# Kernel optimization log

Hardware: AMD Instinct MI355X
Metric: run time of the kernel (lower is better)

## Reference

```python
import jax, jax.numpy as jnp
import numpy as np

UAV_DIM, TASK_DIM = 32, 32
E, H, HID = 128, 4, 256
B, U, T = 16, 64, 128
ENC_H = 128  # encoder hidden width


def _mlp3(x, w0, b0, w1, b1, w2, b2):
    # Linear->ReLU->Linear->ReLU->Linear (weights stored as (in,out))
    x = jax.nn.relu(x @ w0 + b0)
    x = jax.nn.relu(x @ w1 + b1)
    return x @ w2 + b2


def setup_inputs() -> dict:
    key = jax.random.key(0)
    ks = jax.random.split(key, 20)
    s = lambda fan_in: 1.0 / np.sqrt(fan_in)
    d = {
        'uav_feat': jax.random.normal(ks[0], (B, U, UAV_DIM), jnp.float32),
        'task_feat': jax.random.normal(ks[1], (B, T, TASK_DIM), jnp.float32),
        # UAV encoder
        'uw0': jax.random.normal(ks[2], (UAV_DIM, ENC_H), jnp.float32) * s(UAV_DIM),
        'ub0': jnp.zeros((ENC_H,), jnp.float32),
        'uw1': jax.random.normal(ks[3], (ENC_H, ENC_H), jnp.float32) * s(ENC_H),
        'ub1': jnp.zeros((ENC_H,), jnp.float32),
        'uw2': jax.random.normal(ks[4], (ENC_H, E), jnp.float32) * s(ENC_H),
        'ub2': jnp.zeros((E,), jnp.float32),
        # Task encoder
        'tw0': jax.random.normal(ks[5], (TASK_DIM, ENC_H), jnp.float32) * s(TASK_DIM),
        'tb0': jnp.zeros((ENC_H,), jnp.float32),
        'tw1': jax.random.normal(ks[6], (ENC_H, ENC_H), jnp.float32) * s(ENC_H),
        'tb1': jnp.zeros((ENC_H,), jnp.float32),
        'tw2': jax.random.normal(ks[7], (ENC_H, E), jnp.float32) * s(ENC_H),
        'tb2': jnp.zeros((E,), jnp.float32),
        # head queries + fusion MLP (fw1 is the (2E,HID) first linear)
        'head_q': jax.random.normal(ks[8], (H, E), jnp.float32),
        'fw1': jax.random.normal(ks[9], (2 * E, HID), jnp.float32) * s(2 * E),
        'fb1': jnp.zeros((HID,), jnp.float32),
        'fw2': jax.random.normal(ks[10], (HID, 1), jnp.float32) * s(HID),
        'fb2': jnp.zeros((1,), jnp.float32),
    }
    return d


def reference(uav_feat, task_feat, uw0, ub0, uw1, ub1, uw2, ub2,
              tw0, tb0, tw1, tb1, tw2, tb2, head_q, fw1, fb1, fw2, fb2):
    ue = _mlp3(uav_feat, uw0, ub0, uw1, ub1, uw2, ub2)   # (B,U,E)
    te = _mlp3(task_feat, tw0, tb0, tw1, tb1, tw2, tb2)  # (B,T,E)
    # q = uav_embed + per-head query: (B,H,U,E)
    q = ue[:, None, :, :] + head_q[None, :, None, :]
    # Split cat([q,k]) @ fw1 into q@fw1[:E] + k@fw1[E:] — same math, no 2E concat
    qh = jnp.einsum('bhue,ed->bhud', q, fw1[:E])          # (B,H,U,HID)
    kh = jnp.einsum('bte,ed->btd', te, fw1[E:])           # (B,T,HID)
    pre = qh[:, :, :, None, :] + kh[:, None, None, :, :] + fb1  # (B,H,U,T,HID)
    h = jax.nn.relu(pre)
    logits = jnp.einsum('bhutd,do->bhuto', h, fw2)[..., 0] + fb2[0]  # (B,H,U,T)
    return logits
```

## Files before the change

### kernel.cpp

```cpp
#include <hip/hip_runtime.h>
#include <hip/hip_bf16.h>

#define B_ 16
#define U_ 64
#define T_ 128
#define H_ 4
#define E_ 128
#define HID_ 256

typedef _Float16 half_t;
typedef _Float16 h2 __attribute__((ext_vector_type(2)));

__device__ __forceinline__ h2 u2h(unsigned u){ h2 r; __builtin_memcpy(&r, &u, 4); return r; }
__device__ __forceinline__ unsigned pkh(float a, float b){
  h2 r; r.x = (_Float16)a; r.y = (_Float16)b;
  unsigned u; __builtin_memcpy(&u, &r, 4); return u;
}

#define ENC_R 8

__device__ __forceinline__ void layer128(const float (*in)[128], float (*out)[128],
    const float* __restrict__ W, const float* __restrict__ Bb, int j, bool do_relu)
{
  float a[ENC_R];
  float bb = Bb[j];
  #pragma unroll
  for (int r=0;r<ENC_R;r++) a[r]=bb;
  #pragma unroll
  for (int ic=0; ic<4; ic++){
    float w[32];
    #pragma unroll
    for (int i=0;i<32;i++) w[i]=W[(ic*32+i)*128 + j];
    #pragma unroll
    for (int r=0;r<ENC_R;r++){
      float s=0.f;
      #pragma unroll
      for (int i=0;i<32;i++) s = fmaf(in[r][ic*32+i], w[i], s);
      a[r]+=s;
    }
  }
  #pragma unroll
  for (int r=0;r<ENC_R;r++) out[r][j] = do_relu ? fmaxf(a[r],0.f) : a[r];
}

__global__ __launch_bounds__(128) void enc_kernel(
  const float* __restrict__ uav, const float* __restrict__ task,
  const float* __restrict__ uw0, const float* __restrict__ ub0,
  const float* __restrict__ uw1, const float* __restrict__ ub1,
  const float* __restrict__ uw2, const float* __restrict__ ub2,
  const float* __restrict__ tw0, const float* __restrict__ tb0,
  const float* __restrict__ tw1, const float* __restrict__ tb1,
  const float* __restrict__ tw2, const float* __restrict__ tb2,
  const float* __restrict__ headq, const float* __restrict__ fw1,
  float* __restrict__ ueW, half_t* __restrict__ Kg, float* __restrict__ QhW)
{
  __shared__ float X[ENC_R][32];
  __shared__ float Ha[ENC_R][128];
  __shared__ float Hb[ENC_R][128];
  const int j = threadIdx.x;
  const int blk = blockIdx.x;

  const float *w0=nullptr,*b0=nullptr,*w1=nullptr,*b1=nullptr,*w2=nullptr,*b2=nullptr,*xin=nullptr;
  const float* fwbase;
  float* outF = nullptr;
  half_t* outB = nullptr;
  bool only_last = false;
  int row0;

  if (blk < 128) {
    row0 = blk*ENC_R;
    xin = uav + row0*32;
    w0=uw0;b0=ub0;w1=uw1;b1=ub1;w2=uw2;b2=ub2;
    fwbase = fw1;
    outF = ueW + row0*HID_;
  } else if (blk < 384) {
    row0 = (blk-128)*ENC_R;
    xin = task + row0*32;
    w0=tw0;b0=tb0;w1=tw1;b1=tb1;w2=tw2;b2=tb2;
    fwbase = fw1 + 128*HID_;
    outB = Kg + row0*HID_;
  } else {
    only_last = true;
    fwbase = fw1;
    outF = QhW;
  }

  if (!only_last) {
    for (int idx=j; idx<ENC_R*32; idx+=128){ int r=idx>>5, i=idx&31; X[r][i]=xin[idx]; }
    __syncthreads();
    {
      float w[32];
      #pragma unroll
      for (int i=0;i<32;i++) w[i]=w0[i*128 + j];
      float bb=b0[j];
      #pragma unroll
      for (int r=0;r<ENC_R;r++){
        float a=bb;
        #pragma unroll
        for (int i=0;i<32;i++) a = fmaf(X[r][i], w[i], a);
        Ha[r][j]=fmaxf(a,0.f);
      }
    }
    __syncthreads();
    layer128(Ha,Hb,w1,b1,j,true);
    __syncthreads();
    layer128(Hb,Ha,w2,b2,j,false);
    __syncthreads();
  } else {
    #pragma unroll
    for (int r=0;r<4;r++) Ha[r][j] = headq[r*128 + j];
    __syncthreads();
  }

  #pragma unroll
  for (int o=0;o<2;o++){
    const int jo = o*128 + j;
    float a[ENC_R];
    #pragma unroll
    for (int r=0;r<ENC_R;r++) a[r]=0.f;
    #pragma unroll
    for (int ic=0; ic<4; ic++){
      float w[32];
      #pragma unroll
      for (int i=0;i<32;i++) w[i]=fwbase[(ic*32+i)*HID_ + jo];
      #pragma unroll
      for (int r=0;r<ENC_R;r++){
        float s=0.f;
        #pragma unroll
        for (int i=0;i<32;i++) s = fmaf(Ha[r][ic*32+i], w[i], s);
        a[r]+=s;
      }
    }
    if (!only_last) {
      if (outF) {
        #pragma unroll
        for (int r=0;r<ENC_R;r++) outF[r*HID_ + jo] = a[r];
      } else {
        #pragma unroll
        for (int r=0;r<ENC_R;r++) outB[r*HID_ + jo] = (half_t)a[r];
      }
    } else {
      #pragma unroll
      for (int r=0;r<4;r++) outF[r*HID_ + jo] = a[r];
    }
  }
}

#define UTILE 8

__global__ __launch_bounds__(256) void logits_kernel(
  const float* __restrict__ ueW, const float* __restrict__ QhW,
  const half_t* __restrict__ Kg,
  const float* __restrict__ fb1, const float* __restrict__ fw2,
  const float* __restrict__ fb2, float* __restrict__ out)
{
  __shared__ uint4 Kl4[64*32];
  __shared__ uint4 baseb[UTILE][32];
  __shared__ uint4 w2b[32];

  const int tid = threadIdx.x;
  const int wv = tid >> 6;
  const int lane = tid & 63;
  const int b = blockIdx.z, h = blockIdx.y;
  const int u0 = blockIdx.x * UTILE;

  {
    const int u = tid >> 5;
    const int c = tid & 31;
    const float4* ue4 = (const float4*)(ueW + (b*U_ + u0 + u)*HID_);
    const float4* q4  = (const float4*)(QhW + h*HID_);
    const float4* f4  = (const float4*)fb1;
    float4 a0 = ue4[2*c],   a1 = ue4[2*c+1];
    float4 b0 = q4[2*c],    b1 = q4[2*c+1];
    float4 c0 = f4[2*c],    c1 = f4[2*c+1];
    uint4 pv;
    pv.x = pkh(a0.x+b0.x+c0.x, a0.y+b0.y+c0.y);
    pv.y = pkh(a0.z+b0.z+c0.z, a0.w+b0.w+c0.w);
    pv.z = pkh(a1.x+b1.x+c1.x, a1.y+b1.y+c1.y);
    pv.w = pkh(a1.z+b1.z+c1.z, a1.w+b1.w+c1.w);
    baseb[u][c] = pv;
    if (tid < 32) {
      const float4* w4 = (const float4*)fw2;
      float4 w0 = w4[2*tid], w1 = w4[2*tid+1];
      uint4 wv4;
      wv4.x = pkh(w0.x, w0.y); wv4.y = pkh(w0.z, w0.w);
      wv4.z = pkh(w1.x, w1.y); wv4.w = pkh(w1.z, w1.w);
      w2b[tid] = wv4;
    }
  }
  const float fb2f = fb2[0];
  const uint4* Kgp = (const uint4*)(Kg + (size_t)b*T_*HID_);

  const int r0 = wv*2;
  const h2 hz = (h2)((_Float16)0);

  for (int s=0; s<2; s++){
    const int t0 = s*64;
    if (s) __syncthreads();
    for (int i = tid; i < 64*32; i += 256){
      const int t = i >> 5, c = i & 31;
      Kl4[t*32 + ((c + t)&31)] = Kgp[(t0 + t)*32 + c];
    }
    __syncthreads();
    const uint4* myrow = Kl4 + lane*32;
    float acc0 = 0.f, acc1 = 0.f;
    #pragma unroll
    for (int c=0; c<32; c++){
      const uint4 kv = myrow[(c + lane)&31];
      const uint4 w4 = w2b[c];
      const uint4 p0 = baseb[r0][c];
      const uint4 p1 = baseb[r0+1][c];
      h2 x;
      x = __builtin_elementwise_max(u2h(p0.x)+u2h(kv.x), hz);
      acc0 = __builtin_amdgcn_fdot2(x, u2h(w4.x), acc0, false);
      x = __builtin_elementwise_max(u2h(p0.y)+u2h(kv.y), hz);
      acc0 = __builtin_amdgcn_fdot2(x, u2h(w4.y), acc0, false);
      x = __builtin_elementwise_max(u2h(p0.z)+u2h(kv.z), hz);
      acc0 = __builtin_amdgcn_fdot2(x, u2h(w4.z), acc0, false);
      x = __builtin_elementwise_max(u2h(p0.w)+u2h(kv.w), hz);
      acc0 = __builtin_amdgcn_fdot2(x, u2h(w4.w), acc0, false);
      x = __builtin_elementwise_max(u2h(p1.x)+u2h(kv.x), hz);
      acc1 = __builtin_amdgcn_fdot2(x, u2h(w4.x), acc1, false);
      x = __builtin_elementwise_max(u2h(p1.y)+u2h(kv.y), hz);
      acc1 = __builtin_amdgcn_fdot2(x, u2h(w4.y), acc1, false);
      x = __builtin_elementwise_max(u2h(p1.z)+u2h(kv.z), hz);
      acc1 = __builtin_amdgcn_fdot2(x, u2h(w4.z), acc1, false);
      x = __builtin_elementwise_max(u2h(p1.w)+u2h(kv.w), hz);
      acc1 = __builtin_amdgcn_fdot2(x, u2h(w4.w), acc1, false);
    }
    const int t = t0 + lane;
    out[((b*H_ + h)*U_ + (u0 + r0    ))*T_ + t] = acc0 + fb2f;
    out[((b*H_ + h)*U_ + (u0 + r0 + 1))*T_ + t] = acc1 + fb2f;
  }
}

extern "C" void kernel_launch(void* const* d_in, const int* in_sizes, int n_in,
                              void* d_out, int out_size, void* d_ws, size_t ws_size,
                              hipStream_t stream)
{
  const float* uav  = (const float*)d_in[0];
  const float* task = (const float*)d_in[1];
  const float* uw0=(const float*)d_in[2];  const float* ub0=(const float*)d_in[3];
  const float* uw1=(const float*)d_in[4];  const float* ub1=(const float*)d_in[5];
  const float* uw2=(const float*)d_in[6];  const float* ub2=(const float*)d_in[7];
  const float* tw0=(const float*)d_in[8];  const float* tb0=(const float*)d_in[9];
  const float* tw1=(const float*)d_in[10]; const float* tb1=(const float*)d_in[11];
  const float* tw2=(const float*)d_in[12]; const float* tb2=(const float*)d_in[13];
  const float* headq=(const float*)d_in[14];
  const float* fw1=(const float*)d_in[15];
  const float* fb1=(const float*)d_in[16];
  const float* fw2=(const float*)d_in[17];
  const float* fb2=(const float*)d_in[18];

  float* ws  = (float*)d_ws;
  float* ueW = ws;
  float* QhW = ws + 1024*256;
  half_t* Kg = (half_t*)(ws + 1024*256 + 4*256);

  float* out = (float*)d_out;

  hipLaunchKernelGGL(enc_kernel, dim3(385), dim3(128), 0, stream,
      uav, task, uw0,ub0,uw1,ub1,uw2,ub2, tw0,tb0,tw1,tb1,tw2,tb2, headq, fw1,
      ueW, Kg, QhW);
  hipLaunchKernelGGL(logits_kernel, dim3(U_/UTILE, H_, B_), dim3(256), 0, stream,
      ueW, QhW, Kg, fb1, fw2, fb2, out);
}
```

Measured before the change: 130.9 us.

## Run encoder MLPs and fw1 projections on MFMA with fp16 transposed weights

Replaces the scalar FP32 encoder kernel with a prep kernel and an MFMA-based encoder. The prep kernel transposes the weights to fp16 and computes the head-query projection. The encoder then runs the three MLP layers plus the fw1 projection for 64-row tiles using 16x16x32 f16 MFMA with weights staged in LDS. This is meant to cut the encoder's FMA-bound time, at the cost of an extra launch, fp16 rounding of intermediate activations, and only 48 blocks to spread across the device.

```diff
diff --git a/kernel.cpp b/kernel.cpp
--- a/kernel.cpp
+++ b/kernel.cpp
@@ -10,6 +10,8 @@
 
 typedef _Float16 half_t;
 typedef _Float16 h2 __attribute__((ext_vector_type(2)));
+typedef _Float16 f16x8 __attribute__((ext_vector_type(8)));
+typedef float f32x4 __attribute__((ext_vector_type(4)));
 
 __device__ __forceinline__ h2 u2h(unsigned u){ h2 r; __builtin_memcpy(&r, &u, 4); return r; }
 __device__ __forceinline__ unsigned pkh(float a, float b){
@@ -17,131 +19,179 @@
   unsigned u; __builtin_memcpy(&u, &r, 4); return u;
 }
 
-#define ENC_R 8
-
-__device__ __forceinline__ void layer128(const float (*in)[128], float (*out)[128],
-    const float* __restrict__ W, const float* __restrict__ Bb, int j, bool do_relu)
-{
-  float a[ENC_R];
-  float bb = Bb[j];
+__global__ __launch_bounds__(256) void prep_kernel(
+  const float* __restrict__ uw0, const float* __restrict__ uw1, const float* __restrict__ uw2,
+  const float* __restrict__ tw0, const float* __restrict__ tw1, const float* __restrict__ tw2,
+  const float* __restrict__ fw1, const float* __restrict__ headq,
+  half_t* __restrict__ u0t, half_t* __restrict__ u1t, half_t* __restrict__ u2t,
+  half_t* __restrict__ t0t, half_t* __restrict__ t1t, half_t* __restrict__ t2t,
+  half_t* __restrict__ f1at, half_t* __restrict__ f1bt, float* __restrict__ QhW)
+{
+  const int tid = threadIdx.x;
+  const int b = blockIdx.x;
+  if (b == 34) {
+    const int n = tid;
+    float acc[4] = {0.f,0.f,0.f,0.f};
+    for (int e=0;e<128;e++){
+      float w = fw1[e*256 + n];
+      #pragma unroll
+      for (int h=0;h<4;h++) acc[h] = fmaf(headq[h*128+e], w, acc[h]);
+    }
+    #pragma unroll
+    for (int h=0;h<4;h++) QhW[h*256+n] = acc[h];
+    return;
+  }
+  const float* src; int srcStride, row0, col0; half_t* dst; int dstStride, nOff, kOff;
+  if (b < 9) {
+    if (b==0){ src=uw0; row0=0;        dst=u0t; dstStride=32;  kOff=0; }
+    else if (b<5){ src=uw1; row0=(b-1)*32; dst=u1t; dstStride=128; kOff=row0; }
+    else { src=uw2; row0=(b-5)*32; dst=u2t; dstStride=128; kOff=row0; }
+    srcStride=128; col0=0; nOff=0;
+  } else if (b < 18) {
+    int bb=b-9;
+    if (bb==0){ src=tw0; row0=0;        dst=t0t; dstStride=32;  kOff=0; }
+    else if (bb<5){ src=tw1; row0=(bb-1)*32; dst=t1t; dstStride=128; kOff=row0; }
+    else { src=tw2; row0=(bb-5)*32; dst=t2t; dstStride=128; kOff=row0; }
+    srcStride=128; col0=0; nOff=0;
+  } else if (b < 26) {
+    int idx=b-18, kc=idx&3, nc=idx>>2;
+    src=fw1; srcStride=256; row0=kc*32; col0=nc*128;
+    dst=f1at; dstStride=128; kOff=kc*32; nOff=col0;
+  } else {
+    int idx=b-26, kc=idx&3, nc=idx>>2;
+    src=fw1; srcStride=256; row0=128+kc*32; col0=nc*128;
+    dst=f1bt; dstStride=128; kOff=kc*32; nOff=col0;
+  }
+  __shared__ half_t tl[128][33];
   #pragma unroll
-  for (int r=0;r<ENC_R;r++) a[r]=bb;
+  for (int i=0;i<16;i++){ int idx=i*256+tid; int k=idx>>7, n=idx&127;
+    tl[n][k] = (half_t)src[(row0+k)*srcStride + col0 + n]; }
+  __syncthreads();
   #pragma unroll
-  for (int ic=0; ic<4; ic++){
-    float w[32];
-    #pragma unroll
-    for (int i=0;i<32;i++) w[i]=W[(ic*32+i)*128 + j];
-    #pragma unroll
-    for (int r=0;r<ENC_R;r++){
-      float s=0.f;
+  for (int i=0;i<16;i++){ int idx=i*256+tid; int n=idx>>5, k=idx&31;
+    dst[(nOff+n)*dstStride + kOff + k] = tl[n][k]; }
+}
+
+#define PITCH 136
+
+template<int KTILES, int NTILES, bool RELU>
+__device__ __forceinline__ void layer_mfma(const half_t* __restrict__ in,
+    const half_t* __restrict__ W, const float* __restrict__ bias,
+    half_t* __restrict__ out, int m0, int quad, int l16)
+{
+  f16x8 bfrag[KTILES];
+  const half_t* ip = in + (m0+l16)*PITCH + quad*8;
+  #pragma unroll
+  for (int kk=0;kk<KTILES;kk++) bfrag[kk] = *(const f16x8*)(ip + kk*32);
+  #pragma unroll
+  for (int nt=0; nt<NTILES; nt++){
+    f32x4 acc = {0.f,0.f,0.f,0.f};
+    const half_t* wp = W + (nt*16+l16)*PITCH + quad*8;
+    #pragma unroll
+    for (int kk=0;kk<KTILES;kk++){
+      f16x8 a = *(const f16x8*)(wp + kk*32);
+      acc = __builtin_amdgcn_mfma_f32_16x16x32_f16(a, bfrag[kk], acc, 0, 0, 0);
+    }
+    const int n0 = nt*16 + quad*4;
+    const float4 bv = *(const float4*)(bias + n0);
+    float bvr[4] = {bv.x, bv.y, bv.z, bv.w};
+    union { half_t h[4]; uint2 u; } pv;
+    #pragma unroll
+    for (int r=0;r<4;r++){
+      float x = acc[r] + bvr[r];
+      if (RELU) x = fmaxf(x, 0.f);
+      pv.h[r] = (half_t)x;
+    }
+    *(uint2*)(out + (m0+l16)*PITCH + n0) = pv.u;
+  }
+}
+
+__global__ __launch_bounds__(256) void enc_mfma(
+  const float* __restrict__ uav, const float* __restrict__ task,
+  const float* __restrict__ ub0, const float* __restrict__ ub1, const float* __restrict__ ub2,
+  const float* __restrict__ tb0, const float* __restrict__ tb1, const float* __restrict__ tb2,
+  const half_t* __restrict__ u0t, const half_t* __restrict__ u1t, const half_t* __restrict__ u2t,
+  const half_t* __restrict__ t0t, const half_t* __restrict__ t1t, const half_t* __restrict__ t2t,
+  const half_t* __restrict__ f1at, const half_t* __restrict__ f1bt,
+  float* __restrict__ ueW, half_t* __restrict__ Kg)
+{
+  __shared__ half_t Wb[256*PITCH];
+  __shared__ half_t actA[64*PITCH];
+  __shared__ half_t actB[64*PITCH];
+  const int tid = threadIdx.x, lane = tid&63, wv = tid>>6;
+  const int quad = lane>>4, l16 = lane&15;
+  const int m0 = wv*16;
+  const bool isU = blockIdx.x < 16;
+  const int rows0 = (isU ? blockIdx.x : blockIdx.x - 16) * 64;
+  const float* Xsrc = (isU ? uav : task) + rows0*32;
+  const half_t* W0 = isU ? u0t : t0t;
+  const half_t* W1 = isU ? u1t : t1t;
+  const half_t* W2 = isU ? u2t : t2t;
+  const half_t* W3 = isU ? f1at : f1bt;
+  const float* bias0 = isU ? ub0 : tb0;
+  const float* bias1 = isU ? ub1 : tb1;
+  const float* bias2 = isU ? ub2 : tb2;
+
+  {
+    const int r = tid>>2, q = tid&3;
+    const float4 v0 = *(const float4*)(Xsrc + r*32 + q*8);
+    const float4 v1 = *(const float4*)(Xsrc + r*32 + q*8 + 4);
+    half_t* d = actA + r*PITCH + q*8;
+    d[0]=(half_t)v0.x; d[1]=(half_t)v0.y; d[2]=(half_t)v0.z; d[3]=(half_t)v0.w;
+    d[4]=(half_t)v1.x; d[5]=(half_t)v1.y; d[6]=(half_t)v1.z; d[7]=(half_t)v1.w;
+  }
+  {
+    const uint4* s = (const uint4*)W0;
+    #pragma unroll
+    for (int i=0;i<2;i++){ int idx=i*256+tid; int n=idx>>2, kc=idx&3;
+      *(uint4*)(Wb + n*PITCH + kc*8) = s[idx]; }
+  }
+  __syncthreads();
+  layer_mfma<1,8,true >(actA, Wb, bias0, actB, m0, quad, l16);
+  __syncthreads();
+  { const uint4* s = (const uint4*)W1;
+    #pragma unroll
+    for (int i=0;i<8;i++){ int idx=i*256+tid; int n=idx>>4, kc=idx&15;
+      *(uint4*)(Wb + n*PITCH + kc*8) = s[idx]; } }
+  __syncthreads();
+  layer_mfma<4,8,true >(actB, Wb, bias1, actA, m0, quad, l16);
+  __syncthreads();
+  { const uint4* s = (const uint4*)W2;
+    #pragma unroll
+    for (int i=0;i<8;i++){ int idx=i*256+tid; int n=idx>>4, kc=idx&15;
+      *(uint4*)(Wb + n*PITCH + kc*8) = s[idx]; } }
+  __syncthreads();
+  layer_mfma<4,8,false>(actA, Wb, bias2, actB, m0, quad, l16);
+  __syncthreads();
+  { const uint4* s = (const uint4*)W3;
+    #pragma unroll
+    for (int i=0;i<16;i++){ int idx=i*256+tid; int n=idx>>4, kc=idx&15;
+      *(uint4*)(Wb + n*PITCH + kc*8) = s[idx]; } }
+  __syncthreads();
+  {
+    f16x8 bfrag[4];
+    const half_t* ip = actB + (m0+l16)*PITCH + quad*8;
+    #pragma unroll
+    for (int kk=0;kk<4;kk++) bfrag[kk] = *(const f16x8*)(ip + kk*32);
+    const int grow = rows0 + m0 + l16;
+    #pragma unroll
+    for (int nt=0; nt<16; nt++){
+      f32x4 acc = {0.f,0.f,0.f,0.f};
+      const half_t* wp = Wb + (nt*16+l16)*PITCH + quad*8;
       #pragma unroll
-      for (int i=0;i<32;i++) s = fmaf(in[r][ic*32+i], w[i], s);
-      a[r]+=s;
-    }
-  }
-  #pragma unroll
-  for (int r=0;r<ENC_R;r++) out[r][j] = do_relu ? fmaxf(a[r],0.f) : a[r];
-}
-
-__global__ __launch_bounds__(128) void enc_kernel(
-  const float* __restrict__ uav, const float* __restrict__ task,
-  const float* __restrict__ uw0, const float* __restrict__ ub0,
-  const float* __restrict__ uw1, const float* __restrict__ ub1,
-  const float* __restrict__ uw2, const float* __restrict__ ub2,
-  const float* __restrict__ tw0, const float* __restrict__ tb0,
-  const float* __restrict__ tw1, const float* __restrict__ tb1,
-  const float* __restrict__ tw2, const float* __restrict__ tb2,
-  const float* __restrict__ headq, const float* __restrict__ fw1,
-  float* __restrict__ ueW, half_t* __restrict__ Kg, float* __restrict__ QhW)
-{
-  __shared__ float X[ENC_R][32];
-  __shared__ float Ha[ENC_R][128];
-  __shared__ float Hb[ENC_R][128];
-  const int j = threadIdx.x;
-  const int blk = blockIdx.x;
-
-  const float *w0=nullptr,*b0=nullptr,*w1=nullptr,*b1=nullptr,*w2=nullptr,*b2=nullptr,*xin=nullptr;
-  const float* fwbase;
-  float* outF = nullptr;
-  half_t* outB = nullptr;
-  bool only_last = false;
-  int row0;
-
-  if (blk < 128) {
-    row0 = blk*ENC_R;
-    xin = uav + row0*32;
-    w0=uw0;b0=ub0;w1=uw1;b1=ub1;w2=uw2;b2=ub2;
-    fwbase = fw1;
-    outF = ueW + row0*HID_;
-  } else if (blk < 384) {
-    row0 = (blk-128)*ENC_R;
-    xin = task + row0*32;
-    w0=tw0;b0=tb0;w1=tw1;b1=tb1;w2=tw2;b2=tb2;
-    fwbase = fw1 + 128*HID_;
-    outB = Kg + row0*HID_;
-  } else {
-    only_last = true;
-    fwbase = fw1;
-    outF = QhW;
-  }
-
-  if (!only_last) {
-    for (int idx=j; idx<ENC_R*32; idx+=128){ int r=idx>>5, i=idx&31; X[r][i]=xin[idx]; }
-    __syncthreads();
-    {
-      float w[32];
-      #pragma unroll
-      for (int i=0;i<32;i++) w[i]=w0[i*128 + j];
-      float bb=b0[j];
-      #pragma unroll
-      for (int r=0;r<ENC_R;r++){
-        float a=bb;
-        #pragma unroll
-        for (int i=0;i<32;i++) a = fmaf(X[r][i], w[i], a);
-        Ha[r][j]=fmaxf(a,0.f);
+      for (int kk=0;kk<4;kk++){
+        f16x8 a = *(const f16x8*)(wp + kk*32);
+        acc = __builtin_amdgcn_mfma_f32_16x16x32_f16(a, bfrag[kk], acc, 0, 0, 0);
       }
-    }
-    __syncthreads();
-    layer128(Ha,Hb,w1,b1,j,true);
-    __syncthreads();
-    layer128(Hb,Ha,w2,b2,j,false);
-    __syncthreads();
-  } else {
-    #pragma unroll
-    for (int r=0;r<4;r++) Ha[r][j] = headq[r*128 + j];
-    __syncthreads();
-  }
-
-  #pragma unroll
-  for (int o=0;o<2;o++){
-    const int jo = o*128 + j;
-    float a[ENC_R];
-    #pragma unroll
-    for (int r=0;r<ENC_R;r++) a[r]=0.f;
-    #pragma unroll
-    for (int ic=0; ic<4; ic++){
-      float w[32];
-      #pragma unroll
-      for (int i=0;i<32;i++) w[i]=fwbase[(ic*32+i)*HID_ + jo];
-      #pragma unroll
-      for (int r=0;r<ENC_R;r++){
-        float s=0.f;
-        #pragma unroll
-        for (int i=0;i<32;i++) s = fmaf(Ha[r][ic*32+i], w[i], s);
-        a[r]+=s;
+      const int n0 = nt*16 + quad*4;
+      if (isU){
+        *(float4*)(ueW + grow*256 + n0) = make_float4(acc[0],acc[1],acc[2],acc[3]);
+      } else {
+        union { half_t h[4]; uint2 u; } pv;
+        pv.h[0]=(half_t)acc[0]; pv.h[1]=(half_t)acc[1];
+        pv.h[2]=(half_t)acc[2]; pv.h[3]=(half_t)acc[3];
+        *(uint2*)(Kg + grow*256 + n0) = pv.u;
       }
-    }
-    if (!only_last) {
-      if (outF) {
-        #pragma unroll
-        for (int r=0;r<ENC_R;r++) outF[r*HID_ + jo] = a[r];
-      } else {
-        #pragma unroll
-        for (int r=0;r<ENC_R;r++) outB[r*HID_ + jo] = (half_t)a[r];
-      }
-    } else {
-      #pragma unroll
-      for (int r=0;r<4;r++) outF[r*HID_ + jo] = a[r];
     }
   }
 }
@@ -252,16 +302,27 @@
   const float* fw2=(const float*)d_in[17];
   const float* fb2=(const float*)d_in[18];
 
-  float* ws  = (float*)d_ws;
-  float* ueW = ws;
-  float* QhW = ws + 1024*256;
-  half_t* Kg = (half_t*)(ws + 1024*256 + 4*256);
+  float* ueW = (float*)d_ws;
+  float* QhW = ueW + 262144;
+  half_t* hb = (half_t*)(QhW + 1024);
+  half_t* u0t  = hb;
+  half_t* u1t  = hb + 4096;
+  half_t* u2t  = hb + 20480;
+  half_t* t0t  = hb + 36864;
+  half_t* t1t  = hb + 40960;
+  half_t* t2t  = hb + 57344;
+  half_t* f1at = hb + 73728;
+  half_t* f1bt = hb + 106496;
+  half_t* Kg   = hb + 139264;
 
   float* out = (float*)d_out;
 
-  hipLaunchKernelGGL(enc_kernel, dim3(385), dim3(128), 0, stream,
-      uav, task, uw0,ub0,uw1,ub1,uw2,ub2, tw0,tb0,tw1,tb1,tw2,tb2, headq, fw1,
-      ueW, Kg, QhW);
+  hipLaunchKernelGGL(prep_kernel, dim3(35), dim3(256), 0, stream,
+      uw0, uw1, uw2, tw0, tw1, tw2, fw1, headq,
+      u0t, u1t, u2t, t0t, t1t, t2t, f1at, f1bt, QhW);
+  hipLaunchKernelGGL(enc_mfma, dim3(48), dim3(256), 0, stream,
+      uav, task, ub0, ub1, ub2, tb0, tb1, tb2,
+      u0t, u1t, u2t, t0t, t1t, t2t, f1at, f1bt, ueW, Kg);
   hipLaunchKernelGGL(logits_kernel, dim3(U_/UTILE, H_, B_), dim3(256), 0, stream,
       ueW, QhW, Kg, fb1, fw2, fb2, out);
 }
```

Result: faster. 116.1 us (-11.3%).
